# Kernel tuning notes

Measured on AMD Instinct MI355X. Metric: run time of the kernel, lower is better.

Reference implementation:

```python
import jax, jax.numpy as jnp
import numpy as np

B_, T_, D_MODEL = 2, 2048, 1024
EXPAND, D_STATE, D_CONV, HEADDIM = 2, 128, 4, 64
D_INNER = EXPAND * D_MODEL            # 2048
NHEADS = D_INNER // HEADDIM           # 32
CONV_DIM = D_INNER + 2 * D_STATE      # 2304 (x, B, C share the depthwise conv)
D_IN_PROJ = 2 * D_INNER + 2 * D_STATE + NHEADS  # z, xBC, dt


def _rmsnorm(x, w, eps=1e-5):
    return x * jax.lax.rsqrt(jnp.mean(x * x, axis=-1, keepdims=True) + eps) * w


def setup_inputs() -> dict:
    key = jax.random.key(0)
    ks = jax.random.split(key, 8)
    def s(k, shape, scale=0.02):
        return jax.random.normal(k, shape, jnp.float32) * scale
    x = jax.random.normal(ks[0], (B_, T_, D_MODEL), jnp.float32)
    W_in = s(ks[1], (D_MODEL, D_IN_PROJ))
    conv_w = s(ks[2], (CONV_DIM, D_CONV), 0.1)
    conv_b = jnp.zeros((CONV_DIM,), jnp.float32)
    # dt_bias = softplus^-1(dt_init) with dt in [1e-3, 1e-1], per Mamba init
    dt0 = jax.random.uniform(ks[3], (NHEADS,), minval=1e-3, maxval=1e-1)
    dt_bias = jnp.log(jnp.expm1(dt0))
    A_log = jnp.log(jax.random.uniform(ks[4], (NHEADS,), minval=1.0, maxval=16.0))
    D = jnp.ones((NHEADS,), jnp.float32)
    norm_w = jnp.ones((D_MODEL,), jnp.float32)
    gnorm_w = jnp.ones((D_INNER,), jnp.float32)
    W_out = s(ks[5], (D_INNER, D_MODEL))
    return {"x": x, "W_in": W_in, "conv_w": conv_w, "conv_b": conv_b,
            "dt_bias": dt_bias, "A_log": A_log, "D": D,
            "norm_w": norm_w, "gnorm_w": gnorm_w, "W_out": W_out}


def reference(x, W_in, conv_w, conv_b, dt_bias, A_log, D, norm_w, gnorm_w, W_out):
    res = x
    xn = _rmsnorm(x, norm_w)                       # pre-norm
    zxbcdt = xn @ W_in                             # (B,T,D_IN_PROJ)
    z = zxbcdt[..., :D_INNER]
    xBC = zxbcdt[..., D_INNER:D_INNER + CONV_DIM]
    dt = zxbcdt[..., D_INNER + CONV_DIM:]          # (B,T,H)
    # causal depthwise conv over time on concat(x,B,C)
    inp = jnp.transpose(xBC, (0, 2, 1))            # (B,C,T)
    kern = conv_w[:, None, :]                      # (C,1,K)
    conv = jax.lax.conv_general_dilated(
        inp, kern, window_strides=(1,), padding=[(D_CONV - 1, 0)],
        feature_group_count=CONV_DIM, dimension_numbers=("NCH", "OIH", "NCH"))
    xBC = jax.nn.silu(jnp.transpose(conv, (0, 2, 1)) + conv_b)
    xs = xBC[..., :D_INNER].reshape(B_, T_, NHEADS, HEADDIM)  # (B,T,H,P)
    Bm = xBC[..., D_INNER:D_INNER + D_STATE]       # (B,T,N), ngroups=1
    C = xBC[..., D_INNER + D_STATE:]               # (B,T,N)
    dt = jax.nn.softplus(dt + dt_bias)             # (B,T,H)
    A = -jnp.exp(A_log)                            # (H,)

    def step(h, inps):
        x_t, B_t, C_t, dt_t = inps                 # (B,H,P),(B,N),(B,N),(B,H)
        da = jnp.exp(dt_t * A)                     # (B,H)
        h = h * da[:, :, None, None] + (dt_t[..., None] * x_t)[..., None] * B_t[:, None, None, :]
        y = jnp.einsum("bhpn,bn->bhp", h, C_t) + D[None, :, None] * x_t
        return h, y

    h0 = jnp.zeros((B_, NHEADS, HEADDIM, D_STATE), x.dtype)
    seq = (jnp.moveaxis(xs, 1, 0), jnp.moveaxis(Bm, 1, 0),
           jnp.moveaxis(C, 1, 0), jnp.moveaxis(dt, 1, 0))
    _, ys = jax.lax.scan(step, h0, seq)            # ys: (T,B,H,P)
    y = jnp.moveaxis(ys, 0, 1).reshape(B_, T_, D_INNER)
    y = _rmsnorm(y * jax.nn.silu(z), gnorm_w)      # gated RMSNorm
    return y @ W_out + res
```

## Files before the change

kernel.cpp:

```cpp
#include <hip/hip_runtime.h>
#include <hip/hip_bf16.h>

typedef unsigned short u16;
typedef unsigned int u32;
typedef u16 u16x8 __attribute__((ext_vector_type(8)));
typedef u16 u16x4 __attribute__((ext_vector_type(4)));
typedef __bf16 bf16x8 __attribute__((ext_vector_type(8)));
typedef float f32x4 __attribute__((ext_vector_type(4)));

#define B_SZ 2
#define T_SZ 2048
#define DMODEL 1024
#define DINNER 2048
#define DSTATE 128
#define NHEADS 32
#define HEADDIM 64
#define CONVDIM 2304
#define DINPROJ 4384
#define DINPROJ_P 4480
#define NROWS (B_SZ * T_SZ)
#define L_CH 128
#define NCH 16

__device__ __forceinline__ float bf2f(u16 u) {
    union { float f; u32 i; } v; v.i = ((u32)u) << 16; return v.f;
}
__device__ __forceinline__ u16 f2bf(float f) {
    union { float f; u32 i; } v; v.f = f;
    u32 r = v.i + 0x7FFFu + ((v.i >> 16) & 1u);
    return (u16)(r >> 16);
}
__device__ __forceinline__ bf16x8 ldfrag(const u16* p) {
    return __builtin_bit_cast(bf16x8, *(const u16x8*)p);
}
__device__ __forceinline__ void gload_lds16(const u16* g, u16* l) {
    __builtin_amdgcn_global_load_lds(
        (const __attribute__((address_space(1))) unsigned int*)g,
        (__attribute__((address_space(3))) unsigned int*)l, 16, 0, 0);
}

__device__ void trans_tile(const float* __restrict__ in, u16* __restrict__ out,
                           int K, int N, int n0, int k0)
{
    __shared__ u16 tile[64][72];
    const int tid = threadIdx.x;
#pragma unroll
    for (int r = 0; r < 4; r++) {
        int idx = r * 256 + tid;
        int k = idx >> 4, n4 = (idx & 15) << 2;
        const float* src = &in[(size_t)(k0 + k) * N + n0 + n4];
        float4 v;
        if (n0 + n4 + 3 < N) {
            v = *(const float4*)src;
        } else {
            v.x = (n0 + n4 + 0 < N) ? src[0] : 0.f;
            v.y = (n0 + n4 + 1 < N) ? src[1] : 0.f;
            v.z = (n0 + n4 + 2 < N) ? src[2] : 0.f;
            v.w = (n0 + n4 + 3 < N) ? src[3] : 0.f;
        }
        tile[n4 + 0][k] = f2bf(v.x);
        tile[n4 + 1][k] = f2bf(v.y);
        tile[n4 + 2][k] = f2bf(v.z);
        tile[n4 + 3][k] = f2bf(v.w);
    }
    __syncthreads();
#pragma unroll
    for (int r = 0; r < 2; r++) {
        int idx = r * 256 + tid;
        int n = idx >> 3, k8 = (idx & 7) << 3;
        u16x8 vv = *(const u16x8*)&tile[n][k8];
        *(u16x8*)&out[(size_t)(n0 + n) * K + k0 + k8] = vv;
    }
}

__global__ __launch_bounds__(256) void prep_kernel(
    const float* __restrict__ W_in, u16* __restrict__ W_inT,
    const float* __restrict__ W_out, u16* __restrict__ W_outT,
    const float* __restrict__ x, const float* __restrict__ nw, u16* __restrict__ xn,
    const float* __restrict__ cw, u16* __restrict__ cwT)
{
    const int blk = blockIdx.x;
    const int tid = threadIdx.x;
    if (blk < 1120) {
        trans_tile(W_in, W_inT, DMODEL, DINPROJ, (blk % 70) * 64, (blk / 70) * 64);
    } else if (blk < 1632) {
        int idx = blk - 1120;
        trans_tile(W_out, W_outT, DINNER, DMODEL, (idx % 16) * 64, (idx / 16) * 64);
    } else if (blk < 5728) {
        const int row = blk - 1632;
        float4 v = ((const float4*)(x + (size_t)row * DMODEL))[tid];
        float ss = v.x * v.x + v.y * v.y + v.z * v.z + v.w * v.w;
#pragma unroll
        for (int o = 32; o; o >>= 1) ss += __shfl_xor(ss, o);
        __shared__ float red[4];
        if ((tid & 63) == 0) red[tid >> 6] = ss;
        __syncthreads();
        ss = red[0] + red[1] + red[2] + red[3];
        float sc = rsqrtf(ss / (float)DMODEL + 1e-5f);
        float4 wv = ((const float4*)nw)[tid];
        u16x4 o4;
        o4[0] = f2bf(v.x * sc * wv.x);
        o4[1] = f2bf(v.y * sc * wv.y);
        o4[2] = f2bf(v.z * sc * wv.z);
        o4[3] = f2bf(v.w * sc * wv.w);
        *(u16x4*)&xn[(size_t)row * DMODEL + tid * 4] = o4;
    } else {
        for (int idx = tid; idx < 4 * CONVDIM; idx += 256) {
            int k = idx / CONVDIM, c = idx - k * CONVDIM;
            cwT[idx] = f2bf(cw[c * 4 + k]);
        }
    }
}

template<int KC>
__global__ __launch_bounds__(512, 2) void gemm256_kernel(
    const u16* __restrict__ A, const u16* __restrict__ BT, u16* __restrict__ C,
    int Nst, int Brows, int nbn)
{
    __shared__ u16 As[2 * 256 * 64];
    __shared__ u16 Bs[2 * 256 * 64];
    const int tid = threadIdx.x;
    const int l = tid & 63, w = tid >> 6;
    const int wm = w >> 2, wn = w & 3;
    const int ml = l & 15, quad = l >> 4;
    const int srow = l >> 3, sgx = (l & 7) ^ srow;

    const int bid = blockIdx.x;
    const int wg = (bid & 7) * (gridDim.x >> 3) + (bid >> 3);
    const int m0 = (wg / nbn) * 256;
    const int n0 = (wg % nbn) * 256;
    const int bcap = Brows - 1 - n0;

    const u16* Ag = A + (size_t)m0 * KC;
    const u16* Bg = BT + (size_t)n0 * KC;
    const int NT = KC / 64;

    f32x4 acc[8][4] = {};
    bf16x8 af[4][2];
    bf16x8 bfr[2][2][2];

#define BARX() { asm volatile("" ::: "memory"); __builtin_amdgcn_s_barrier(); asm volatile("" ::: "memory"); }
#define STG(Gp, Lp, bsel, hs, kt, cap)                                        \
    { const int kcol_ = (kt) * 64;                                            \
      _Pragma("unroll")                                                       \
      for (int j_ = 0; j_ < 2; j_++) {                                        \
          const int i0_ = (w * 2 + j_) * 8;                                   \
          const int r0_ = (i0_ & 63) + ((i0_ >> 6) << 7) + ((hs) << 6);       \
          int gr_ = r0_ + srow; if (gr_ > (cap)) gr_ = (cap);                 \
          gload_lds16(Gp + (size_t)gr_ * KC + kcol_ + sgx * 8,                \
                      Lp + (bsel) * 16384 + r0_ * 64);                        \
      } }
#define RDA(bsel, qm)                                                         \
    _Pragma("unroll") for (int mt_ = 0; mt_ < 4; mt_++)                       \
    _Pragma("unroll") for (int ks_ = 0; ks_ < 2; ks_++)                       \
        af[mt_][ks_] = ldfrag(&As[(bsel) * 16384 +                            \
            (wm * 128 + ((qm) * 4 + mt_) * 16 + ml) * 64 +                    \
            (((ks_ * 4 + quad) ^ (ml & 7)) * 8)]);
#define RDB(bsel, qn)                                                         \
    _Pragma("unroll") for (int nt_ = 0; nt_ < 2; nt_++)                       \
    _Pragma("unroll") for (int ks_ = 0; ks_ < 2; ks_++)                       \
        bfr[qn][nt_][ks_] = ldfrag(&Bs[(bsel) * 16384 +                       \
            (wn * 64 + ((qn) * 2 + nt_) * 16 + ml) * 64 +                     \
            (((ks_ * 4 + quad) ^ (ml & 7)) * 8)]);
#define MMA(qm, qn)                                                           \
    __builtin_amdgcn_s_setprio(1);                                            \
    _Pragma("unroll") for (int ks_ = 0; ks_ < 2; ks_++)                       \
    _Pragma("unroll") for (int mt_ = 0; mt_ < 4; mt_++)                       \
    _Pragma("unroll") for (int nt_ = 0; nt_ < 2; nt_++)                       \
        acc[(qm) * 4 + mt_][(qn) * 2 + nt_] =                                 \
            __builtin_amdgcn_mfma_f32_16x16x32_bf16(                          \
                af[mt_][ks_], bfr[qn][nt_][ks_],                              \
                acc[(qm) * 4 + mt_][(qn) * 2 + nt_], 0, 0, 0);                \
    __builtin_amdgcn_s_setprio(0);

    STG(Ag, As, 0, 0, 0, 255);
    STG(Bg, Bs, 0, 0, 0, bcap);
    STG(Bg, Bs, 0, 1, 0, bcap);
    STG(Ag, As, 0, 1, 0, bcap < 255 ? bcap : 255);
    STG(Ag, As, 1, 0, 1, 255);
    STG(Bg, Bs, 1, 0, 1, bcap);
    asm volatile("s_waitcnt vmcnt(4)" ::: "memory");
    BARX();

#define TILE(t, bsel)                                                         \
    { const bool s1_ = (t) + 1 < NT, s2_ = (t) + 2 < NT;                      \
      RDA(bsel, 0); RDB(bsel, 0);                                             \
      if (s1_) STG(Bg, Bs, (bsel) ^ 1, 1, (t) + 1, bcap);                     \
      BARX(); MMA(0, 0); BARX();                                              \
      RDB(bsel, 1);                                                           \
      if (s1_) STG(Ag, As, (bsel) ^ 1, 1, (t) + 1, 255);                      \
      BARX(); MMA(0, 1); BARX();                                              \
      RDA(bsel, 1);                                                           \
      if (s2_) STG(Ag, As, bsel, 0, (t) + 2, 255);                            \
      BARX(); MMA(1, 0); BARX();                                              \
      if (s2_) { STG(Bg, Bs, bsel, 0, (t) + 2, bcap);                         \
                 asm volatile("s_waitcnt vmcnt(4)" ::: "memory"); }           \
      else     { asm volatile("s_waitcnt vmcnt(0)" ::: "memory"); }           \
      BARX(); MMA(1, 1); BARX(); }

#pragma unroll 1
    for (int t = 0; t < NT; t += 2) {
        TILE(t, 0);
        TILE(t + 1, 1);
    }
#undef TILE
#undef MMA
#undef RDB
#undef RDA
#undef STG
#undef BARX

#pragma unroll
    for (int mt = 0; mt < 8; mt++)
#pragma unroll
        for (int nt = 0; nt < 4; nt++)
#pragma unroll
            for (int rg = 0; rg < 4; rg++) {
                int m = m0 + wm * 128 + mt * 16 + quad * 4 + rg;
                int n = n0 + wn * 64 + nt * 16 + ml;
                if (n < Nst)
                    C[(size_t)m * Nst + n] = f2bf(acc[mt][nt][rg]);
            }
}


template<int KC, int MODE>
__global__ __launch_bounds__(256) void gemm128x64_kernel(
    const u16* __restrict__ A, const u16* __restrict__ BT, void* __restrict__ Cv,
    const float* __restrict__ Res, int Nst, int Nlim)
{
    __shared__ u16 As[128 * 64];
    __shared__ u16 Bs[64 * 64];
    const int tid = threadIdx.x;
    const int l = tid & 63, w = tid >> 6;
    const int m0 = blockIdx.y * 128;
    const int n0 = blockIdx.x * 64;
    const int ml = l & 15, quad = l >> 4;
    const int wm = w * 32;
    f32x4 acc[2][4] = {};
    const int srow = l >> 3;
    const int sgx = (l & 7) ^ srow;
    const u16* Ag = A + (size_t)(m0 + w * 8 + srow) * KC + sgx * 8;
    const u16* Bg = BT + (size_t)(n0 + w * 8 + srow) * KC + sgx * 8;
    u16* const As_w = &As[(w * 8) * 64];
    u16* const Bs_w = &Bs[(w * 8) * 64];

#pragma unroll 4
    for (int k0 = 0; k0 < KC; k0 += 64) {
        __syncthreads();
#pragma unroll
        for (int j = 0; j < 4; j++)
            gload_lds16(Ag + (size_t)(j * 32) * KC + k0, As_w + j * 32 * 64);
#pragma unroll
        for (int j = 0; j < 2; j++)
            gload_lds16(Bg + (size_t)(j * 32) * KC + k0, Bs_w + j * 32 * 64);
        __syncthreads();
#pragma unroll
        for (int ks4 = 0; ks4 < 2; ks4++) {
            bf16x8 af[2], bfr[4];
#pragma unroll
            for (int i = 0; i < 2; i++)
                af[i] = ldfrag(&As[(wm + i * 16 + ml) * 64 +
                                   (((ks4 * 4 + quad) ^ (ml & 7)) * 8)]);
#pragma unroll
            for (int i = 0; i < 4; i++)
                bfr[i] = ldfrag(&Bs[(i * 16 + ml) * 64 +
                                    (((ks4 * 4 + quad) ^ (ml & 7)) * 8)]);
#pragma unroll
            for (int mt = 0; mt < 2; mt++)
#pragma unroll
                for (int nt = 0; nt < 4; nt++)
                    acc[mt][nt] = __builtin_amdgcn_mfma_f32_16x16x32_bf16(
                        af[mt], bfr[nt], acc[mt][nt], 0, 0, 0);
        }
    }
#pragma unroll
    for (int mt = 0; mt < 2; mt++)
#pragma unroll
        for (int nt = 0; nt < 4; nt++)
#pragma unroll
            for (int rg = 0; rg < 4; rg++) {
                int m = m0 + wm + mt * 16 + quad * 4 + rg;
                int n = n0 + nt * 16 + ml;
                if (n < Nlim) {
                    if (MODE == 0)
                        ((u16*)Cv)[(size_t)m * Nst + n] = f2bf(acc[mt][nt][rg]);
                    else
                        ((float*)Cv)[(size_t)m * Nst + n] =
                            acc[mt][nt][rg] + Res[(size_t)m * Nst + n];
                }
            }
}

#define NGRAN (CONVDIM / 8)
__global__ __launch_bounds__(256) void conv_silu_kernel(
    const u16* __restrict__ zx, const u16* __restrict__ cwT,
    const float* __restrict__ cb, const float* __restrict__ dt_bias,
    u16* __restrict__ out, float* __restrict__ dts)
{
    int idx = blockIdx.x * 256 + threadIdx.x;
    if (idx < B_SZ * NHEADS * T_SZ) {
        int t = idx & (T_SZ - 1);
        int bh = idx >> 11;
        int h = bh & 31, b = bh >> 5;
        float v = bf2f(zx[(size_t)(b * T_SZ + t) * DINPROJ + (DINNER + CONVDIM) + h]) + dt_bias[h];
        float sp = (v > 20.f) ? v : log1pf(expf(v));
        dts[((size_t)bh << 11) + t] = sp;
    }
    int gr = idx % NGRAN;
    int bt = idx / NGRAN;
    int t = bt & (T_SZ - 1);
    int c0 = gr * 8;
    float acc[8];
#pragma unroll
    for (int u = 0; u < 8; u++) acc[u] = cb[c0 + u];
    const u16* base = zx + (size_t)bt * DINPROJ + DINNER + c0;
#pragma unroll
    for (int k = 0; k < 4; k++) {
        int tt = t - 3 + k;
        if (tt >= 0) {
            u16x8 xv = *(const u16x8*)(base + (ptrdiff_t)(k - 3) * DINPROJ);
            u16x8 wv = *(const u16x8*)&cwT[k * CONVDIM + c0];
#pragma unroll
            for (int u = 0; u < 8; u++)
                acc[u] += bf2f(xv[u]) * bf2f(wv[u]);
        }
    }
    u16 res[8];
#pragma unroll
    for (int u = 0; u < 8; u++) {
        float s = acc[u] / (1.f + expf(-acc[u]));
        res[u] = f2bf(s);
    }
    *(u16x8*)&out[(size_t)bt * CONVDIM + c0] = *(u16x8*)res;
}

__global__ __launch_bounds__(256) void chunk_state_kernel(
    const u16* __restrict__ xbc, const float* __restrict__ dts_g,
    const float* __restrict__ A_log, float* __restrict__ cs_g, u16* __restrict__ S_bf)
{
    const int g = blockIdx.x;
    const int b = g >> 9, rem = g & 511, c = rem >> 5, h = rem & 31;
    const int tid = threadIdx.x;
    __shared__ float tmp[128], dt_l[128], d2e[128];
    __shared__ u16 Xw[64][136];
    __shared__ u16 BsT[128][136];
    const float A = -__expf(A_log[h]);
    if (tid < 128) {
        float d = dts_g[(((size_t)(b * 32 + h)) << 11) + (c << 7) + tid];
        dt_l[tid] = d; tmp[tid] = d * A;
    }
    __syncthreads();
    for (int off = 1; off < 128; off <<= 1) {
        float add = 0.f;
        if (tid < 128 && tid >= off) add = tmp[tid - off];
        __syncthreads();
        if (tid < 128) tmp[tid] += add;
        __syncthreads();
    }
    if (tid < 128) {
        float cs = tmp[tid];
        cs_g[(((size_t)(b * 32 + h)) << 11) + (c << 7) + tid] = cs;
        d2e[tid] = __expf(tmp[127] - cs) * dt_l[tid];
    }
    __syncthreads();
    const size_t rowbase = ((size_t)(b * T_SZ + c * L_CH)) * CONVDIM;
#pragma unroll
    for (int r = 0; r < 4; r++) {
        int v = tid + r * 256;
        int t = v >> 3, p0 = (v & 7) << 3;
        u16x8 xv = *(const u16x8*)&xbc[rowbase + (size_t)t * CONVDIM + h * 64 + p0];
        float s = d2e[t];
#pragma unroll
        for (int u = 0; u < 8; u++) Xw[p0 + u][t] = f2bf(bf2f(xv[u]) * s);
    }
#pragma unroll
    for (int r = 0; r < 8; r++) {
        int v = tid + r * 256;
        int t = v >> 4, n0 = (v & 15) << 3;
        u16x8 bv = *(const u16x8*)&xbc[rowbase + (size_t)t * CONVDIM + DINNER + n0];
#pragma unroll
        for (int u = 0; u < 8; u++) BsT[n0 + u][t] = bv[u];
    }
    __syncthreads();
    const int lane = tid & 63, wv = tid >> 6, ml = lane & 15, quad = lane >> 4;
    f32x4 acc[8] = {};
    for (int k0 = 0; k0 < 128; k0 += 32) {
        bf16x8 af = ldfrag(&Xw[wv * 16 + ml][k0 + quad * 8]);
#pragma unroll
        for (int nt = 0; nt < 8; nt++) {
            bf16x8 bf = ldfrag(&BsT[nt * 16 + ml][k0 + quad * 8]);
            acc[nt] = __builtin_amdgcn_mfma_f32_16x16x32_bf16(af, bf, acc[nt], 0, 0, 0);
        }
    }
    const size_t base = (size_t)g * 8192;
#pragma unroll
    for (int nt = 0; nt < 8; nt++) {
#pragma unroll
        for (int rg = 0; rg < 4; rg++) {
            int p = wv * 16 + quad * 4 + rg, n = nt * 16 + ml;
            S_bf[base + p * 128 + n] = f2bf(acc[nt][rg]);
        }
    }
}

__global__ __launch_bounds__(256) void state_pass_kernel(
    const float* __restrict__ cs_g, u16* __restrict__ S_bf)
{
    const int bh = blockIdx.x >> 3, b = bh >> 5, h = bh & 31;
    const int off = (blockIdx.x & 7) * 1024 + threadIdx.x * 4;
    const float* csb = cs_g + (((size_t)(b * 32 + h)) << 11);
    float H[4] = {0.f, 0.f, 0.f, 0.f};
    for (int c = 0; c < NCH; c++) {
        float decay = __expf(csb[(c << 7) + 127]);
        size_t slot = ((size_t)((b * NCH + c) * 32 + h)) * 8192 + off;
        u16x4 tv = *(const u16x4*)&S_bf[slot];
        u16x4 hw;
#pragma unroll
        for (int i = 0; i < 4; i++) hw[i] = f2bf(H[i]);
        *(u16x4*)&S_bf[slot] = hw;
#pragma unroll
        for (int i = 0; i < 4; i++) H[i] = H[i] * decay + bf2f(tv[i]);
    }
}

__global__ __launch_bounds__(256) void chunk_out_kernel(
    const u16* __restrict__ xbc, const float* __restrict__ dts_g,
    const float* __restrict__ cs_g, const u16* __restrict__ H_bf,
    const float* __restrict__ Dv, u16* __restrict__ yraw)
{
    const int g = blockIdx.x;
    const int b = g >> 9, rem = g & 511, c = rem >> 5, h = rem & 31;
    const int tid = threadIdx.x;
    __shared__ u16 Xs[64][136];
    __shared__ u16 Gs[128][40];
    __shared__ float cs_l[128], P_l[128], dt_l[128];
    const size_t rowbase = ((size_t)(b * T_SZ + c * L_CH)) * CONVDIM;
    const u16* Cg = xbc + rowbase + DINNER + 128;
    const u16* Bg = xbc + rowbase + DINNER;
    const u16* Hg = H_bf + (size_t)g * 8192;
    if (tid < 128) {
        float cs = cs_g[(((size_t)(b * 32 + h)) << 11) + (c << 7) + tid];
        cs_l[tid] = cs; P_l[tid] = __expf(cs);
        dt_l[tid] = dts_g[(((size_t)(b * 32 + h)) << 11) + (c << 7) + tid];
    }
#pragma unroll
    for (int r = 0; r < 4; r++) {
        int v = tid + r * 256; int t = v >> 3, p0 = (v & 7) << 3;
        u16x8 xv = *(const u16x8*)&xbc[rowbase + (size_t)t * CONVDIM + h * 64 + p0];
#pragma unroll
        for (int u = 0; u < 8; u++) Xs[p0 + u][t] = xv[u];
    }
    __syncthreads();
    const int lane = tid & 63, wv = tid >> 6, ml = lane & 15, quad = lane >> 4;
    const int trow = wv * 32;
    f32x4 accY[2][4] = {};
    for (int k0 = 0; k0 < 128; k0 += 32) {
        bf16x8 af0 = ldfrag(Cg + (size_t)(trow + ml) * CONVDIM + k0 + quad * 8);
        bf16x8 af1 = ldfrag(Cg + (size_t)(trow + 16 + ml) * CONVDIM + k0 + quad * 8);
#pragma unroll
        for (int pt = 0; pt < 4; pt++) {
            bf16x8 bf = ldfrag(Hg + (pt * 16 + ml) * 128 + k0 + quad * 8);
            accY[0][pt] = __builtin_amdgcn_mfma_f32_16x16x32_bf16(af0, bf, accY[0][pt], 0, 0, 0);
            accY[1][pt] = __builtin_amdgcn_mfma_f32_16x16x32_bf16(af1, bf, accY[1][pt], 0, 0, 0);
        }
    }
#pragma unroll
    for (int mt = 0; mt < 2; mt++) {
#pragma unroll
        for (int rg = 0; rg < 4; rg++) {
            float pp = P_l[trow + mt * 16 + quad * 4 + rg];
#pragma unroll
            for (int pt = 0; pt < 4; pt++) accY[mt][pt][rg] *= pp;
        }
    }
    for (int js = 0; js < 4; js++) {
        const int j0 = js * 32;
        f32x4 Ga[2][2] = {};
        for (int k0 = 0; k0 < 128; k0 += 32) {
            bf16x8 af0 = ldfrag(Cg + (size_t)(trow + ml) * CONVDIM + k0 + quad * 8);
            bf16x8 af1 = ldfrag(Cg + (size_t)(trow + 16 + ml) * CONVDIM + k0 + quad * 8);
            bf16x8 bf0 = ldfrag(Bg + (size_t)(j0 + ml) * CONVDIM + k0 + quad * 8);
            bf16x8 bf1 = ldfrag(Bg + (size_t)(j0 + 16 + ml) * CONVDIM + k0 + quad * 8);
            Ga[0][0] = __builtin_amdgcn_mfma_f32_16x16x32_bf16(af0, bf0, Ga[0][0], 0, 0, 0);
            Ga[0][1] = __builtin_amdgcn_mfma_f32_16x16x32_bf16(af0, bf1, Ga[0][1], 0, 0, 0);
            Ga[1][0] = __builtin_amdgcn_mfma_f32_16x16x32_bf16(af1, bf0, Ga[1][0], 0, 0, 0);
            Ga[1][1] = __builtin_amdgcn_mfma_f32_16x16x32_bf16(af1, bf1, Ga[1][1], 0, 0, 0);
        }
#pragma unroll
        for (int mt = 0; mt < 2; mt++) {
#pragma unroll
            for (int jt = 0; jt < 2; jt++) {
#pragma unroll
                for (int rg = 0; rg < 4; rg++) {
                    int t = trow + mt * 16 + quad * 4 + rg;
                    int j = j0 + jt * 16 + ml;
                    float val = 0.f;
                    if (t >= j) val = Ga[mt][jt][rg] * __expf(cs_l[t] - cs_l[j]) * dt_l[j];
                    Gs[t][jt * 16 + ml] = f2bf(val);
                }
            }
        }
#pragma unroll
        for (int mt = 0; mt < 2; mt++) {
            bf16x8 af = ldfrag(&Gs[trow + mt * 16 + ml][quad * 8]);
#pragma unroll
            for (int pt = 0; pt < 4; pt++) {
                bf16x8 bf = ldfrag(&Xs[pt * 16 + ml][j0 + quad * 8]);
                accY[mt][pt] = __builtin_amdgcn_mfma_f32_16x16x32_bf16(af, bf, accY[mt][pt], 0, 0, 0);
            }
        }
    }
    const float Dh = Dv[h];
    const size_t ybase = ((size_t)(b * T_SZ + c * L_CH)) * DINNER;
#pragma unroll
    for (int mt = 0; mt < 2; mt++) {
#pragma unroll
        for (int pt = 0; pt < 4; pt++) {
#pragma unroll
            for (int rg = 0; rg < 4; rg++) {
                int t = trow + mt * 16 + quad * 4 + rg;
                int p = pt * 16 + ml;
                float v = accY[mt][pt][rg] + Dh * bf2f(Xs[p][t]);
                yraw[ybase + (size_t)t * DINNER + h * 64 + p] = f2bf(v);
            }
        }
    }
}

__global__ __launch_bounds__(256) void postnorm_kernel(
    const u16* __restrict__ yraw, const u16* __restrict__ zx,
    const float* __restrict__ gw, u16* __restrict__ out)
{
    const int row = blockIdx.x;
    const int tid = threadIdx.x;
    u16x8 yv = *(const u16x8*)(yraw + (size_t)row * DINNER + tid * 8);
    u16x8 zv = *(const u16x8*)(zx + (size_t)row * DINPROJ + tid * 8);
    float vals[8]; float ss = 0.f;
#pragma unroll
    for (int i = 0; i < 8; i++) {
        float y = bf2f(yv[i]);
        float z = bf2f(zv[i]);
        float s = z / (1.f + expf(-z));
        float t = y * s; vals[i] = t; ss += t * t;
    }
#pragma unroll
    for (int o = 32; o; o >>= 1) ss += __shfl_xor(ss, o);
    __shared__ float red[4];
    if ((tid & 63) == 0) red[tid >> 6] = ss;
    __syncthreads();
    ss = red[0] + red[1] + red[2] + red[3];
    float sc = rsqrtf(ss / (float)DINNER + 1e-5f);
    u16 o8[8];
#pragma unroll
    for (int i = 0; i < 8; i++) o8[i] = f2bf(vals[i] * sc * gw[tid * 8 + i]);
    *(u16x8*)(out + (size_t)row * DINNER + tid * 8) = *(u16x8*)o8;
}

extern "C" void kernel_launch(void* const* d_in, const int* in_sizes, int n_in,
                              void* d_out, int out_size, void* d_ws, size_t ws_size,
                              hipStream_t stream) {
    const float* x       = (const float*)d_in[0];
    const float* W_in    = (const float*)d_in[1];
    const float* conv_w  = (const float*)d_in[2];
    const float* conv_b  = (const float*)d_in[3];
    const float* dt_bias = (const float*)d_in[4];
    const float* A_log   = (const float*)d_in[5];
    const float* Dv      = (const float*)d_in[6];
    const float* norm_w  = (const float*)d_in[7];
    const float* gnorm_w = (const float*)d_in[8];
    const float* W_out   = (const float*)d_in[9];
    float* out = (float*)d_out;

    char* ws = (char*)d_ws;
    u16*   xn    = (u16*)(ws);
    u16*   W_inT = (u16*)(ws + 8388608);
    u16*   S_bf  = (u16*)(ws);
    float* cs_g  = (float*)(ws + 16777216);
    u16*   zx    = (u16*)(ws + 17563648);
    u16*   xbc   = (u16*)(ws + 53477376);
    float* dts   = (float*)(ws + 72351744);
    u16*   yraw  = (u16*)(ws + 72876032);
    u16*   cwT   = (u16*)(ws + 89653248);
    u16*   W_outT= (u16*)(ws + 89671680);
    u16*   ynorm = yraw;

    prep_kernel<<<5729, 256, 0, stream>>>(
        W_in, W_inT, W_out, W_outT, x, norm_w, xn, conv_w, cwT);
    gemm256_kernel<DMODEL><<<256, 512, 0, stream>>>(
        xn, W_inT, zx, DINPROJ, DINPROJ_P, 16);
    gemm128x64_kernel<DMODEL, 0><<<dim3(5, NROWS / 128), 256, 0, stream>>>(
        xn, W_inT + (size_t)4096 * DMODEL, zx + 4096, nullptr,
        DINPROJ, DINPROJ - 4096);
    conv_silu_kernel<<<(NROWS * NGRAN) / 256, 256, 0, stream>>>(
        zx, cwT, conv_b, dt_bias, xbc, dts);
    chunk_state_kernel<<<B_SZ * NCH * NHEADS, 256, 0, stream>>>(xbc, dts, A_log, cs_g, S_bf);
    state_pass_kernel<<<B_SZ * NHEADS * 8, 256, 0, stream>>>(cs_g, S_bf);
    chunk_out_kernel<<<B_SZ * NCH * NHEADS, 256, 0, stream>>>(xbc, dts, cs_g, S_bf, Dv, yraw);
    postnorm_kernel<<<NROWS, 256, 0, stream>>>(yraw, zx, gnorm_w, ynorm);
    gemm128x64_kernel<DINNER, 1><<<dim3(DMODEL / 64, NROWS / 128), 256, 0, stream>>>(
        ynorm, W_outT, out, x, DMODEL, DMODEL);
}
```

Measured before the change: 285.5 us.

## Swap MFMA operands for packed row-wise epilogue stores and add 128x128 out-proj GEMM

Swaps the A/B operands of the MFMA instructions across the GEMMs and the SSM chunk kernels, so each lane holds four consecutive columns of one output row. This allows packed 4-element bf16 and float4 stores instead of scattered scalar stores. The output projection moves to a new 128x128-tile kernel with a vectorised residual add. In chunk_out, the C fragments are hoisted into registers and reused across the inner loops. The trade-offs are higher register pressure and the removal of the column bound check in the large GEMM epilogue, which now writes padded columns past the logical width.

```diff
diff --git a/kernel.cpp b/kernel.cpp
--- a/kernel.cpp
+++ b/kernel.cpp
@@ -169,14 +169,14 @@
     _Pragma("unroll") for (int nt_ = 0; nt_ < 2; nt_++)                       \
         acc[(qm) * 4 + mt_][(qn) * 2 + nt_] =                                 \
             __builtin_amdgcn_mfma_f32_16x16x32_bf16(                          \
-                af[mt_][ks_], bfr[qn][nt_][ks_],                              \
+                bfr[qn][nt_][ks_], af[mt_][ks_],                              \
                 acc[(qm) * 4 + mt_][(qn) * 2 + nt_], 0, 0, 0);                \
     __builtin_amdgcn_s_setprio(0);
 
     STG(Ag, As, 0, 0, 0, 255);
     STG(Bg, Bs, 0, 0, 0, bcap);
     STG(Bg, Bs, 0, 1, 0, bcap);
-    STG(Ag, As, 0, 1, 0, bcap < 255 ? bcap : 255);
+    STG(Ag, As, 0, 1, 0, 255);
     STG(Ag, As, 1, 0, 1, 255);
     STG(Bg, Bs, 1, 0, 1, bcap);
     asm volatile("s_waitcnt vmcnt(4)" ::: "memory");
@@ -211,23 +211,23 @@
 #undef BARX
 
 #pragma unroll
-    for (int mt = 0; mt < 8; mt++)
-#pragma unroll
-        for (int nt = 0; nt < 4; nt++)
-#pragma unroll
-            for (int rg = 0; rg < 4; rg++) {
-                int m = m0 + wm * 128 + mt * 16 + quad * 4 + rg;
-                int n = n0 + wn * 64 + nt * 16 + ml;
-                if (n < Nst)
-                    C[(size_t)m * Nst + n] = f2bf(acc[mt][nt][rg]);
-            }
-}
-
-
-template<int KC, int MODE>
+    for (int mt = 0; mt < 8; mt++) {
+        const int m = m0 + wm * 128 + mt * 16 + ml;
+#pragma unroll
+        for (int nt = 0; nt < 4; nt++) {
+            const int nb = n0 + wn * 64 + nt * 16 + quad * 4;
+            u16x4 pk;
+#pragma unroll
+            for (int rg = 0; rg < 4; rg++) pk[rg] = f2bf(acc[mt][nt][rg]);
+            *(u16x4*)&C[(size_t)m * Nst + nb] = pk;
+        }
+    }
+}
+
+template<int KC>
 __global__ __launch_bounds__(256) void gemm128x64_kernel(
-    const u16* __restrict__ A, const u16* __restrict__ BT, void* __restrict__ Cv,
-    const float* __restrict__ Res, int Nst, int Nlim)
+    const u16* __restrict__ A, const u16* __restrict__ BT, u16* __restrict__ C,
+    int Nst, int Nlim)
 {
     __shared__ u16 As[128 * 64];
     __shared__ u16 Bs[64 * 64];
@@ -271,25 +271,89 @@
 #pragma unroll
                 for (int nt = 0; nt < 4; nt++)
                     acc[mt][nt] = __builtin_amdgcn_mfma_f32_16x16x32_bf16(
-                        af[mt], bfr[nt], acc[mt][nt], 0, 0, 0);
-        }
-    }
-#pragma unroll
-    for (int mt = 0; mt < 2; mt++)
-#pragma unroll
-        for (int nt = 0; nt < 4; nt++)
-#pragma unroll
-            for (int rg = 0; rg < 4; rg++) {
-                int m = m0 + wm + mt * 16 + quad * 4 + rg;
-                int n = n0 + nt * 16 + ml;
-                if (n < Nlim) {
-                    if (MODE == 0)
-                        ((u16*)Cv)[(size_t)m * Nst + n] = f2bf(acc[mt][nt][rg]);
-                    else
-                        ((float*)Cv)[(size_t)m * Nst + n] =
-                            acc[mt][nt][rg] + Res[(size_t)m * Nst + n];
-                }
+                        bfr[nt], af[mt], acc[mt][nt], 0, 0, 0);
+        }
+    }
+#pragma unroll
+    for (int mt = 0; mt < 2; mt++) {
+        const int m = m0 + wm + mt * 16 + ml;
+#pragma unroll
+        for (int nt = 0; nt < 4; nt++) {
+            const int nb = n0 + nt * 16 + quad * 4;
+            if (nb < Nlim) {
+                u16x4 pk;
+#pragma unroll
+                for (int rg = 0; rg < 4; rg++) pk[rg] = f2bf(acc[mt][nt][rg]);
+                *(u16x4*)&C[(size_t)m * Nst + nb] = pk;
             }
+        }
+    }
+}
+
+template<int KC>
+__global__ __launch_bounds__(256) void gemm128_res_kernel(
+    const u16* __restrict__ A, const u16* __restrict__ BT, float* __restrict__ C,
+    const float* __restrict__ Res, int Nst)
+{
+    __shared__ u16 As[128 * 64];
+    __shared__ u16 Bs[128 * 64];
+    const int tid = threadIdx.x;
+    const int l = tid & 63, w = tid >> 6;
+    const int m0 = blockIdx.y * 128;
+    const int n0 = blockIdx.x * 128;
+    const int ml = l & 15, quad = l >> 4;
+    const int wm = (w & 1) * 64, wn = (w >> 1) * 64;
+    f32x4 acc[4][4] = {};
+    const int srow = l >> 3;
+    const int sgx = (l & 7) ^ srow;
+    const u16* Ag = A + (size_t)(m0 + w * 8 + srow) * KC + sgx * 8;
+    const u16* Bg = BT + (size_t)(n0 + w * 8 + srow) * KC + sgx * 8;
+    u16* const As_w = &As[(w * 8) * 64];
+    u16* const Bs_w = &Bs[(w * 8) * 64];
+
+#pragma unroll 4
+    for (int k0 = 0; k0 < KC; k0 += 64) {
+        __syncthreads();
+#pragma unroll
+        for (int j = 0; j < 4; j++) {
+            gload_lds16(Ag + (size_t)(j * 32) * KC + k0, As_w + j * 32 * 64);
+            gload_lds16(Bg + (size_t)(j * 32) * KC + k0, Bs_w + j * 32 * 64);
+        }
+        __syncthreads();
+#pragma unroll
+        for (int ks4 = 0; ks4 < 2; ks4++) {
+            bf16x8 af[4], bfr[4];
+#pragma unroll
+            for (int i = 0; i < 4; i++)
+                af[i] = ldfrag(&As[(wm + i * 16 + ml) * 64 +
+                                   (((ks4 * 4 + quad) ^ (ml & 7)) * 8)]);
+#pragma unroll
+            for (int i = 0; i < 4; i++)
+                bfr[i] = ldfrag(&Bs[(wn + i * 16 + ml) * 64 +
+                                    (((ks4 * 4 + quad) ^ (ml & 7)) * 8)]);
+#pragma unroll
+            for (int mt = 0; mt < 4; mt++)
+#pragma unroll
+                for (int nt = 0; nt < 4; nt++)
+                    acc[mt][nt] = __builtin_amdgcn_mfma_f32_16x16x32_bf16(
+                        bfr[nt], af[mt], acc[mt][nt], 0, 0, 0);
+        }
+    }
+#pragma unroll
+    for (int mt = 0; mt < 4; mt++) {
+        const int m = m0 + wm + mt * 16 + ml;
+#pragma unroll
+        for (int nt = 0; nt < 4; nt++) {
+            const int nb = n0 + wn + nt * 16 + quad * 4;
+            float4 r = *(const float4*)&Res[(size_t)m * Nst + nb];
+            float4 o;
+            o.x = acc[mt][nt][0] + r.x;
+            o.y = acc[mt][nt][1] + r.y;
+            o.z = acc[mt][nt][2] + r.z;
+            o.w = acc[mt][nt][3] + r.w;
+            *(float4*)&C[(size_t)m * Nst + nb] = o;
+        }
+    }
 }
 
 #define NGRAN (CONVDIM / 8)
@@ -390,17 +454,18 @@
 #pragma unroll
         for (int nt = 0; nt < 8; nt++) {
             bf16x8 bf = ldfrag(&BsT[nt * 16 + ml][k0 + quad * 8]);
-            acc[nt] = __builtin_amdgcn_mfma_f32_16x16x32_bf16(af, bf, acc[nt], 0, 0, 0);
+            acc[nt] = __builtin_amdgcn_mfma_f32_16x16x32_bf16(bf, af, acc[nt], 0, 0, 0);
         }
     }
     const size_t base = (size_t)g * 8192;
+    const int p = wv * 16 + ml;
 #pragma unroll
     for (int nt = 0; nt < 8; nt++) {
-#pragma unroll
-        for (int rg = 0; rg < 4; rg++) {
-            int p = wv * 16 + quad * 4 + rg, n = nt * 16 + ml;
-            S_bf[base + p * 128 + n] = f2bf(acc[nt][rg]);
-        }
+        const int nb = nt * 16 + quad * 4;
+        u16x4 pk;
+#pragma unroll
+        for (int rg = 0; rg < 4; rg++) pk[rg] = f2bf(acc[nt][rg]);
+        *(u16x4*)&S_bf[base + p * 128 + nb] = pk;
     }
 }
 
@@ -454,60 +519,66 @@
     __syncthreads();
     const int lane = tid & 63, wv = tid >> 6, ml = lane & 15, quad = lane >> 4;
     const int trow = wv * 32;
+    bf16x8 cf[2][4];
+#pragma unroll
+    for (int mt = 0; mt < 2; mt++)
+#pragma unroll
+        for (int kk = 0; kk < 4; kk++)
+            cf[mt][kk] = ldfrag(Cg + (size_t)(trow + mt * 16 + ml) * CONVDIM + kk * 32 + quad * 8);
     f32x4 accY[2][4] = {};
-    for (int k0 = 0; k0 < 128; k0 += 32) {
-        bf16x8 af0 = ldfrag(Cg + (size_t)(trow + ml) * CONVDIM + k0 + quad * 8);
-        bf16x8 af1 = ldfrag(Cg + (size_t)(trow + 16 + ml) * CONVDIM + k0 + quad * 8);
+#pragma unroll
+    for (int kk = 0; kk < 4; kk++) {
 #pragma unroll
         for (int pt = 0; pt < 4; pt++) {
-            bf16x8 bf = ldfrag(Hg + (pt * 16 + ml) * 128 + k0 + quad * 8);
-            accY[0][pt] = __builtin_amdgcn_mfma_f32_16x16x32_bf16(af0, bf, accY[0][pt], 0, 0, 0);
-            accY[1][pt] = __builtin_amdgcn_mfma_f32_16x16x32_bf16(af1, bf, accY[1][pt], 0, 0, 0);
+            bf16x8 bf = ldfrag(Hg + (pt * 16 + ml) * 128 + kk * 32 + quad * 8);
+            accY[0][pt] = __builtin_amdgcn_mfma_f32_16x16x32_bf16(bf, cf[0][kk], accY[0][pt], 0, 0, 0);
+            accY[1][pt] = __builtin_amdgcn_mfma_f32_16x16x32_bf16(bf, cf[1][kk], accY[1][pt], 0, 0, 0);
         }
     }
 #pragma unroll
     for (int mt = 0; mt < 2; mt++) {
-#pragma unroll
-        for (int rg = 0; rg < 4; rg++) {
-            float pp = P_l[trow + mt * 16 + quad * 4 + rg];
-#pragma unroll
-            for (int pt = 0; pt < 4; pt++) accY[mt][pt][rg] *= pp;
-        }
+        const float pp = P_l[trow + mt * 16 + ml];
+#pragma unroll
+        for (int pt = 0; pt < 4; pt++)
+#pragma unroll
+            for (int rg = 0; rg < 4; rg++) accY[mt][pt][rg] *= pp;
     }
     for (int js = 0; js < 4; js++) {
         const int j0 = js * 32;
         f32x4 Ga[2][2] = {};
-        for (int k0 = 0; k0 < 128; k0 += 32) {
-            bf16x8 af0 = ldfrag(Cg + (size_t)(trow + ml) * CONVDIM + k0 + quad * 8);
-            bf16x8 af1 = ldfrag(Cg + (size_t)(trow + 16 + ml) * CONVDIM + k0 + quad * 8);
-            bf16x8 bf0 = ldfrag(Bg + (size_t)(j0 + ml) * CONVDIM + k0 + quad * 8);
-            bf16x8 bf1 = ldfrag(Bg + (size_t)(j0 + 16 + ml) * CONVDIM + k0 + quad * 8);
-            Ga[0][0] = __builtin_amdgcn_mfma_f32_16x16x32_bf16(af0, bf0, Ga[0][0], 0, 0, 0);
-            Ga[0][1] = __builtin_amdgcn_mfma_f32_16x16x32_bf16(af0, bf1, Ga[0][1], 0, 0, 0);
-            Ga[1][0] = __builtin_amdgcn_mfma_f32_16x16x32_bf16(af1, bf0, Ga[1][0], 0, 0, 0);
-            Ga[1][1] = __builtin_amdgcn_mfma_f32_16x16x32_bf16(af1, bf1, Ga[1][1], 0, 0, 0);
+#pragma unroll
+        for (int kk = 0; kk < 4; kk++) {
+            bf16x8 bf0 = ldfrag(Bg + (size_t)(j0 + ml) * CONVDIM + kk * 32 + quad * 8);
+            bf16x8 bf1 = ldfrag(Bg + (size_t)(j0 + 16 + ml) * CONVDIM + kk * 32 + quad * 8);
+            Ga[0][0] = __builtin_amdgcn_mfma_f32_16x16x32_bf16(bf0, cf[0][kk], Ga[0][0], 0, 0, 0);
+            Ga[0][1] = __builtin_amdgcn_mfma_f32_16x16x32_bf16(bf1, cf[0][kk], Ga[0][1], 0, 0, 0);
+            Ga[1][0] = __builtin_amdgcn_mfma_f32_16x16x32_bf16(bf0, cf[1][kk], Ga[1][0], 0, 0, 0);
+            Ga[1][1] = __builtin_amdgcn_mfma_f32_16x16x32_bf16(bf1, cf[1][kk], Ga[1][1], 0, 0, 0);
         }
 #pragma unroll
         for (int mt = 0; mt < 2; mt++) {
+            const int t = trow + mt * 16 + ml;
+            const float cst = cs_l[t];
 #pragma unroll
             for (int jt = 0; jt < 2; jt++) {
+                u16x4 pk;
 #pragma unroll
                 for (int rg = 0; rg < 4; rg++) {
-                    int t = trow + mt * 16 + quad * 4 + rg;
-                    int j = j0 + jt * 16 + ml;
+                    int j = j0 + jt * 16 + quad * 4 + rg;
                     float val = 0.f;
-                    if (t >= j) val = Ga[mt][jt][rg] * __expf(cs_l[t] - cs_l[j]) * dt_l[j];
-                    Gs[t][jt * 16 + ml] = f2bf(val);
+                    if (t >= j) val = Ga[mt][jt][rg] * __expf(cst - cs_l[j]) * dt_l[j];
+                    pk[rg] = f2bf(val);
                 }
+                *(u16x4*)&Gs[t][jt * 16 + quad * 4] = pk;
             }
         }
 #pragma unroll
         for (int mt = 0; mt < 2; mt++) {
-            bf16x8 af = ldfrag(&Gs[trow + mt * 16 + ml][quad * 8]);
+            bf16x8 ag = ldfrag(&Gs[trow + mt * 16 + ml][quad * 8]);
 #pragma unroll
             for (int pt = 0; pt < 4; pt++) {
-                bf16x8 bf = ldfrag(&Xs[pt * 16 + ml][j0 + quad * 8]);
-                accY[mt][pt] = __builtin_amdgcn_mfma_f32_16x16x32_bf16(af, bf, accY[mt][pt], 0, 0, 0);
+                bf16x8 bx = ldfrag(&Xs[pt * 16 + ml][j0 + quad * 8]);
+                accY[mt][pt] = __builtin_amdgcn_mfma_f32_16x16x32_bf16(bx, ag, accY[mt][pt], 0, 0, 0);
             }
         }
     }
@@ -515,15 +586,15 @@
     const size_t ybase = ((size_t)(b * T_SZ + c * L_CH)) * DINNER;
 #pragma unroll
     for (int mt = 0; mt < 2; mt++) {
+        const int t = trow + mt * 16 + ml;
 #pragma unroll
         for (int pt = 0; pt < 4; pt++) {
-#pragma unroll
-            for (int rg = 0; rg < 4; rg++) {
-                int t = trow + mt * 16 + quad * 4 + rg;
-                int p = pt * 16 + ml;
-                float v = accY[mt][pt][rg] + Dh * bf2f(Xs[p][t]);
-                yraw[ybase + (size_t)t * DINNER + h * 64 + p] = f2bf(v);
-            }
+            const int pb = pt * 16 + quad * 4;
+            u16x4 pk;
+#pragma unroll
+            for (int rg = 0; rg < 4; rg++)
+                pk[rg] = f2bf(accY[mt][pt][rg] + Dh * bf2f(Xs[pb + rg][t]));
+            *(u16x4*)&yraw[ybase + (size_t)t * DINNER + h * 64 + pb] = pk;
         }
     }
 }
@@ -589,15 +660,14 @@
         W_in, W_inT, W_out, W_outT, x, norm_w, xn, conv_w, cwT);
     gemm256_kernel<DMODEL><<<256, 512, 0, stream>>>(
         xn, W_inT, zx, DINPROJ, DINPROJ_P, 16);
-    gemm128x64_kernel<DMODEL, 0><<<dim3(5, NROWS / 128), 256, 0, stream>>>(
-        xn, W_inT + (size_t)4096 * DMODEL, zx + 4096, nullptr,
-        DINPROJ, DINPROJ - 4096);
+    gemm128x64_kernel<DMODEL><<<dim3(5, NROWS / 128), 256, 0, stream>>>(
+        xn, W_inT + (size_t)4096 * DMODEL, zx + 4096, DINPROJ, DINPROJ - 4096);
     conv_silu_kernel<<<(NROWS * NGRAN) / 256, 256, 0, stream>>>(
         zx, cwT, conv_b, dt_bias, xbc, dts);
     chunk_state_kernel<<<B_SZ * NCH * NHEADS, 256, 0, stream>>>(xbc, dts, A_log, cs_g, S_bf);
     state_pass_kernel<<<B_SZ * NHEADS * 8, 256, 0, stream>>>(cs_g, S_bf);
     chunk_out_kernel<<<B_SZ * NCH * NHEADS, 256, 0, stream>>>(xbc, dts, cs_g, S_bf, Dv, yraw);
     postnorm_kernel<<<NROWS, 256, 0, stream>>>(yraw, zx, gnorm_w, ynorm);
-    gemm128x64_kernel<DINNER, 1><<<dim3(DMODEL / 64, NROWS / 128), 256, 0, stream>>>(
-        ynorm, W_outT, out, x, DMODEL, DMODEL);
-}
+    gemm128_res_kernel<DINNER><<<dim3(DMODEL / 128, NROWS / 128), 256, 0, stream>>>(
+        ynorm, W_outT, out, x, DMODEL);
+}
```

After: 302.1 us. 5.8% more time.

## Transpose MFMA operands for vectorized epilogue stores and hoist SSD fragment loads

Applied to the files above, without the earlier changes.

Swaps the A/B operands of the MFMA calls in the GEMM kernels and the chunk-state kernel, so each lane holds four consecutive output columns. The epilogues can then write packed 4-element bf16 or float4 stores (with a vectorized residual read) instead of scalar strided stores. In the chunk-scan kernel, the C fragments are loaded once into registers and reused by both the state product and the intra-chunk Gram computation, and the B fragments for the next j-block are prefetched into registers. It also drops a row clamp on one A staging load and the n<Nst bound check in the big GEMM epilogue, which assumes the padded output width covers every write. The cost is higher register pressure from the hoisted fragments.

```diff
diff --git a/kernel.cpp b/kernel.cpp
--- a/kernel.cpp
+++ b/kernel.cpp
@@ -160,7 +160,7 @@
     _Pragma("unroll") for (int nt_ = 0; nt_ < 2; nt_++)                       \
     _Pragma("unroll") for (int ks_ = 0; ks_ < 2; ks_++)                       \
         bfr[qn][nt_][ks_] = ldfrag(&Bs[(bsel) * 16384 +                       \
-            (wn * 64 + ((qn) * 2 + nt_) * 16 + ml) * 64 +                     \
+            (wn * 64 + ((qn) * 2 + nt_) * 16 + ml) * 64 +                    \
             (((ks_ * 4 + quad) ^ (ml & 7)) * 8)]);
 #define MMA(qm, qn)                                                           \
     __builtin_amdgcn_s_setprio(1);                                            \
@@ -169,14 +169,14 @@
     _Pragma("unroll") for (int nt_ = 0; nt_ < 2; nt_++)                       \
         acc[(qm) * 4 + mt_][(qn) * 2 + nt_] =                                 \
             __builtin_amdgcn_mfma_f32_16x16x32_bf16(                          \
-                af[mt_][ks_], bfr[qn][nt_][ks_],                              \
+                bfr[qn][nt_][ks_], af[mt_][ks_],                              \
                 acc[(qm) * 4 + mt_][(qn) * 2 + nt_], 0, 0, 0);                \
     __builtin_amdgcn_s_setprio(0);
 
     STG(Ag, As, 0, 0, 0, 255);
     STG(Bg, Bs, 0, 0, 0, bcap);
     STG(Bg, Bs, 0, 1, 0, bcap);
-    STG(Ag, As, 0, 1, 0, bcap < 255 ? bcap : 255);
+    STG(Ag, As, 0, 1, 0, 255);
     STG(Ag, As, 1, 0, 1, 255);
     STG(Bg, Bs, 1, 0, 1, bcap);
     asm volatile("s_waitcnt vmcnt(4)" ::: "memory");
@@ -211,18 +211,18 @@
 #undef BARX
 
 #pragma unroll
-    for (int mt = 0; mt < 8; mt++)
-#pragma unroll
-        for (int nt = 0; nt < 4; nt++)
-#pragma unroll
-            for (int rg = 0; rg < 4; rg++) {
-                int m = m0 + wm * 128 + mt * 16 + quad * 4 + rg;
-                int n = n0 + wn * 64 + nt * 16 + ml;
-                if (n < Nst)
-                    C[(size_t)m * Nst + n] = f2bf(acc[mt][nt][rg]);
-            }
-}
-
+    for (int mt = 0; mt < 8; mt++) {
+        const int m = m0 + wm * 128 + mt * 16 + ml;
+#pragma unroll
+        for (int nt = 0; nt < 4; nt++) {
+            const int nb = n0 + wn * 64 + nt * 16 + quad * 4;
+            u16x4 pk;
+#pragma unroll
+            for (int rg = 0; rg < 4; rg++) pk[rg] = f2bf(acc[mt][nt][rg]);
+            *(u16x4*)&C[(size_t)m * Nst + nb] = pk;
+        }
+    }
+}
 
 template<int KC, int MODE>
 __global__ __launch_bounds__(256) void gemm128x64_kernel(
@@ -271,25 +271,33 @@
 #pragma unroll
                 for (int nt = 0; nt < 4; nt++)
                     acc[mt][nt] = __builtin_amdgcn_mfma_f32_16x16x32_bf16(
-                        af[mt], bfr[nt], acc[mt][nt], 0, 0, 0);
-        }
-    }
-#pragma unroll
-    for (int mt = 0; mt < 2; mt++)
-#pragma unroll
-        for (int nt = 0; nt < 4; nt++)
-#pragma unroll
-            for (int rg = 0; rg < 4; rg++) {
-                int m = m0 + wm + mt * 16 + quad * 4 + rg;
-                int n = n0 + nt * 16 + ml;
-                if (n < Nlim) {
-                    if (MODE == 0)
-                        ((u16*)Cv)[(size_t)m * Nst + n] = f2bf(acc[mt][nt][rg]);
-                    else
-                        ((float*)Cv)[(size_t)m * Nst + n] =
-                            acc[mt][nt][rg] + Res[(size_t)m * Nst + n];
+                        bfr[nt], af[mt], acc[mt][nt], 0, 0, 0);
+        }
+    }
+#pragma unroll
+    for (int mt = 0; mt < 2; mt++) {
+        const int m = m0 + wm + mt * 16 + ml;
+#pragma unroll
+        for (int nt = 0; nt < 4; nt++) {
+            const int nb = n0 + nt * 16 + quad * 4;
+            if (nb < Nlim) {
+                if (MODE == 0) {
+                    u16x4 pk;
+#pragma unroll
+                    for (int rg = 0; rg < 4; rg++) pk[rg] = f2bf(acc[mt][nt][rg]);
+                    *(u16x4*)&((u16*)Cv)[(size_t)m * Nst + nb] = pk;
+                } else {
+                    float4 r = *(const float4*)&Res[(size_t)m * Nst + nb];
+                    float4 o;
+                    o.x = acc[mt][nt][0] + r.x;
+                    o.y = acc[mt][nt][1] + r.y;
+                    o.z = acc[mt][nt][2] + r.z;
+                    o.w = acc[mt][nt][3] + r.w;
+                    *(float4*)&((float*)Cv)[(size_t)m * Nst + nb] = o;
                 }
             }
+        }
+    }
 }
 
 #define NGRAN (CONVDIM / 8)
@@ -390,17 +398,18 @@
 #pragma unroll
         for (int nt = 0; nt < 8; nt++) {
             bf16x8 bf = ldfrag(&BsT[nt * 16 + ml][k0 + quad * 8]);
-            acc[nt] = __builtin_amdgcn_mfma_f32_16x16x32_bf16(af, bf, acc[nt], 0, 0, 0);
+            acc[nt] = __builtin_amdgcn_mfma_f32_16x16x32_bf16(bf, af, acc[nt], 0, 0, 0);
         }
     }
     const size_t base = (size_t)g * 8192;
+    const int p = wv * 16 + ml;
 #pragma unroll
     for (int nt = 0; nt < 8; nt++) {
-#pragma unroll
-        for (int rg = 0; rg < 4; rg++) {
-            int p = wv * 16 + quad * 4 + rg, n = nt * 16 + ml;
-            S_bf[base + p * 128 + n] = f2bf(acc[nt][rg]);
-        }
+        const int nb = nt * 16 + quad * 4;
+        u16x4 pk;
+#pragma unroll
+        for (int rg = 0; rg < 4; rg++) pk[rg] = f2bf(acc[nt][rg]);
+        *(u16x4*)&S_bf[base + p * 128 + nb] = pk;
     }
 }
 
@@ -454,15 +463,20 @@
     __syncthreads();
     const int lane = tid & 63, wv = tid >> 6, ml = lane & 15, quad = lane >> 4;
     const int trow = wv * 32;
+    bf16x8 cf[2][4];
+#pragma unroll
+    for (int mt = 0; mt < 2; mt++)
+#pragma unroll
+        for (int kk = 0; kk < 4; kk++)
+            cf[mt][kk] = ldfrag(Cg + (size_t)(trow + mt * 16 + ml) * CONVDIM + kk * 32 + quad * 8);
     f32x4 accY[2][4] = {};
-    for (int k0 = 0; k0 < 128; k0 += 32) {
-        bf16x8 af0 = ldfrag(Cg + (size_t)(trow + ml) * CONVDIM + k0 + quad * 8);
-        bf16x8 af1 = ldfrag(Cg + (size_t)(trow + 16 + ml) * CONVDIM + k0 + quad * 8);
+#pragma unroll
+    for (int kk = 0; kk < 4; kk++) {
 #pragma unroll
         for (int pt = 0; pt < 4; pt++) {
-            bf16x8 bf = ldfrag(Hg + (pt * 16 + ml) * 128 + k0 + quad * 8);
-            accY[0][pt] = __builtin_amdgcn_mfma_f32_16x16x32_bf16(af0, bf, accY[0][pt], 0, 0, 0);
-            accY[1][pt] = __builtin_amdgcn_mfma_f32_16x16x32_bf16(af1, bf, accY[1][pt], 0, 0, 0);
+            bf16x8 bf = ldfrag(Hg + (pt * 16 + ml) * 128 + kk * 32 + quad * 8);
+            accY[0][pt] = __builtin_amdgcn_mfma_f32_16x16x32_bf16(cf[0][kk], bf, accY[0][pt], 0, 0, 0);
+            accY[1][pt] = __builtin_amdgcn_mfma_f32_16x16x32_bf16(cf[1][kk], bf, accY[1][pt], 0, 0, 0);
         }
     }
 #pragma unroll
@@ -473,19 +487,29 @@
 #pragma unroll
             for (int pt = 0; pt < 4; pt++) accY[mt][pt][rg] *= pp;
         }
+    }
+    bf16x8 bp[4][2];
+#pragma unroll
+    for (int kk = 0; kk < 4; kk++) {
+        bp[kk][0] = ldfrag(Bg + (size_t)(ml) * CONVDIM + kk * 32 + quad * 8);
+        bp[kk][1] = ldfrag(Bg + (size_t)(16 + ml) * CONVDIM + kk * 32 + quad * 8);
     }
     for (int js = 0; js < 4; js++) {
         const int j0 = js * 32;
         f32x4 Ga[2][2] = {};
-        for (int k0 = 0; k0 < 128; k0 += 32) {
-            bf16x8 af0 = ldfrag(Cg + (size_t)(trow + ml) * CONVDIM + k0 + quad * 8);
-            bf16x8 af1 = ldfrag(Cg + (size_t)(trow + 16 + ml) * CONVDIM + k0 + quad * 8);
-            bf16x8 bf0 = ldfrag(Bg + (size_t)(j0 + ml) * CONVDIM + k0 + quad * 8);
-            bf16x8 bf1 = ldfrag(Bg + (size_t)(j0 + 16 + ml) * CONVDIM + k0 + quad * 8);
-            Ga[0][0] = __builtin_amdgcn_mfma_f32_16x16x32_bf16(af0, bf0, Ga[0][0], 0, 0, 0);
-            Ga[0][1] = __builtin_amdgcn_mfma_f32_16x16x32_bf16(af0, bf1, Ga[0][1], 0, 0, 0);
-            Ga[1][0] = __builtin_amdgcn_mfma_f32_16x16x32_bf16(af1, bf0, Ga[1][0], 0, 0, 0);
-            Ga[1][1] = __builtin_amdgcn_mfma_f32_16x16x32_bf16(af1, bf1, Ga[1][1], 0, 0, 0);
+#pragma unroll
+        for (int kk = 0; kk < 4; kk++) {
+            Ga[0][0] = __builtin_amdgcn_mfma_f32_16x16x32_bf16(cf[0][kk], bp[kk][0], Ga[0][0], 0, 0, 0);
+            Ga[0][1] = __builtin_amdgcn_mfma_f32_16x16x32_bf16(cf[0][kk], bp[kk][1], Ga[0][1], 0, 0, 0);
+            Ga[1][0] = __builtin_amdgcn_mfma_f32_16x16x32_bf16(cf[1][kk], bp[kk][0], Ga[1][0], 0, 0, 0);
+            Ga[1][1] = __builtin_amdgcn_mfma_f32_16x16x32_bf16(cf[1][kk], bp[kk][1], Ga[1][1], 0, 0, 0);
+        }
+        if (js < 3) {
+#pragma unroll
+            for (int kk = 0; kk < 4; kk++) {
+                bp[kk][0] = ldfrag(Bg + (size_t)(j0 + 32 + ml) * CONVDIM + kk * 32 + quad * 8);
+                bp[kk][1] = ldfrag(Bg + (size_t)(j0 + 48 + ml) * CONVDIM + kk * 32 + quad * 8);
+            }
         }
 #pragma unroll
         for (int mt = 0; mt < 2; mt++) {
@@ -503,11 +527,11 @@
         }
 #pragma unroll
         for (int mt = 0; mt < 2; mt++) {
-            bf16x8 af = ldfrag(&Gs[trow + mt * 16 + ml][quad * 8]);
+            bf16x8 ag = ldfrag(&Gs[trow + mt * 16 + ml][quad * 8]);
 #pragma unroll
             for (int pt = 0; pt < 4; pt++) {
-                bf16x8 bf = ldfrag(&Xs[pt * 16 + ml][j0 + quad * 8]);
-                accY[mt][pt] = __builtin_amdgcn_mfma_f32_16x16x32_bf16(af, bf, accY[mt][pt], 0, 0, 0);
+                bf16x8 bx = ldfrag(&Xs[pt * 16 + ml][j0 + quad * 8]);
+                accY[mt][pt] = __builtin_amdgcn_mfma_f32_16x16x32_bf16(ag, bx, accY[mt][pt], 0, 0, 0);
             }
         }
     }
```

After: 285.8 us. Within noise of the previous version (+0.1%).
